# Performance work log

Hardware: AMD Instinct MI355X
Metric: run time of the kernel (lower is better)

Reference implementation:

```python
import jax, jax.numpy as jnp
from jax import lax
import numpy as np

T = 100  # number of binarization thresholds, as in nn.Module (linspace(0,1,100))
THRESHOLDS = jnp.linspace(0.0, 1.0, T)


def _count_components(binimg):
    """4-connected component count per image via iterative min-label propagation.
    binimg: [N,H,W] float in {0,1}. Returns [N] int32 component counts.
    Equivalent math to the source's recursive DFS flood fill, vectorized."""
    N, H, W = binimg.shape
    fg = binimg > 0
    BIG = H * W  # sentinel label for background
    idx = jnp.arange(H * W, dtype=jnp.int32).reshape(H, W)
    lab0 = jnp.where(fg, idx[None], jnp.int32(BIG))

    def prop(lab):
        p = jnp.pad(lab, ((0, 0), (1, 1), (1, 1)), constant_values=BIG)
        nmin = jnp.minimum(jnp.minimum(p[:, :-2, 1:-1], p[:, 2:, 1:-1]),
                           jnp.minimum(p[:, 1:-1, :-2], p[:, 1:-1, 2:]))
        return jnp.where(fg, jnp.minimum(lab, nmin), jnp.int32(BIG))

    def cond(c):
        return ~c[1]

    def body(c):
        lab = c[0]
        new = prop(prop(prop(lab)))  # 3 propagation steps per convergence check
        return (new, jnp.all(new == lab))

    lab, _ = lax.while_loop(cond, body, (lab0, jnp.array(False)))
    # each component keeps exactly one pixel whose label equals its own index
    return jnp.sum(fg & (lab == idx[None]), axis=(1, 2)).astype(jnp.int32)


def _betti(prob):
    """prob: [R,H,W] -> [T,R,2] (b0, b1) per threshold per region.
    b1 = b0 - euler, euler = #pixels - #4-neighbor edges (as in source)."""
    R, H, W = prob.shape
    binz = (prob[None] > THRESHOLDS[:, None, None, None]).astype(jnp.float32)  # [T,R,H,W]
    flat = binz.reshape(T * R, H, W)
    b0 = lax.stop_gradient(_count_components(flat)).astype(jnp.float32).reshape(T, R)
    pix = flat.sum((1, 2))
    edges = (flat[:, :-1] * flat[:, 1:]).sum((1, 2)) + (flat[:, :, :-1] * flat[:, :, 1:]).sum((1, 2))
    euler = (pix - edges).reshape(T, R)
    b1 = b0 - euler
    return jnp.stack([b0, b1], axis=-1)  # [T,R,2]


def setup_inputs() -> dict:
    key = jax.random.key(0)
    k1, k2 = jax.random.split(key)
    three_class_prob = jax.random.uniform(k1, (4, 3, 128, 128), dtype=jnp.float32)
    selected_regions = jnp.arange(4, dtype=jnp.int64)
    gt_barcodes = jax.random.uniform(k2, (4, 6, T - 1, 2), dtype=jnp.float32)
    return {"three_class_prob": three_class_prob,
            "selected_regions": selected_regions,
            "gt_barcodes": gt_barcodes}


def reference(three_class_prob, selected_regions, gt_barcodes):
    sel = three_class_prob[selected_regions]  # [R,3,H,W]
    inside = _betti(sel[:, 0])     # channel 0
    boundary = _betti(sel[:, 1])   # channel 1
    union = inside                 # source uses channel 0:1 again -> same values
    codes = jnp.concatenate([inside, boundary, union], axis=-1)  # [T,R,6]
    # barcode extraction: birth at increases of the betti curve, death at decreases
    d = codes[1:] - codes[:-1]                 # [T-1,R,6]
    th = THRESHOLDS[:-1, None, None]
    birth = jnp.where(d > 0, th, 0.0)
    death = jnp.where(d < 0, th, 0.0)
    barcodes = jnp.stack([birth, death], axis=-1).transpose(1, 2, 0, 3)  # [R,6,T-1,2]
    # fixed-shape matching: pair barcodes sorted by birth time (Hungarian surrogate)
    ord_b = jnp.argsort(barcodes[..., 0], axis=-1)
    ord_g = jnp.argsort(gt_barcodes[..., 0], axis=-1)
    bs = jnp.take_along_axis(barcodes, ord_b[..., None], axis=-2)
    gs = jnp.take_along_axis(gt_barcodes, ord_g[..., None], axis=-2)
    matched_diff = jnp.sum(jnp.abs(bs - gs), axis=-1)                  # [R,6,T-1]
    unmatched_len = jnp.sum(barcodes[..., 1] - barcodes[..., 0], axis=-1)  # [R,6]
    return jnp.mean(matched_diff) + jnp.mean(unmatched_len)
```

## Files before the change

kernel.cpp:

```cpp
#include <hip/hip_runtime.h>

typedef unsigned long long u64;

__device__ __forceinline__ int find_root(int* L, int a){
    int p = L[a];
    while(p != a){
        int gp = L[p];
        if(gp != p) L[a] = gp;
        a = p; p = gp;
    }
    return a;
}

__device__ __forceinline__ int unite(int* L, int a, int b){
    while(true){
        a = find_root(L, a);
        b = find_root(L, b);
        if(a == b) return 0;
        int hi = (a > b) ? a : b;
        int lo = (a > b) ? b : a;
        int old = atomicCAS(&L[hi], hi, lo);
        if(old == hi) return 1;
        a = old; b = lo;
    }
}

__global__ __launch_bounds__(256) void ccl_kernel(const float* __restrict__ prob,
                                                  const int*   __restrict__ sel,
                                                  float*       __restrict__ betti,
                                                  float*       __restrict__ out){
    __shared__ u64 M[256];
    __shared__ u64 S[256];
    __shared__ int Pr[257];
    __shared__ int L[8192];
    __shared__ int red[12];
    const int tid = threadIdx.x, bid = blockIdx.x;
    if(bid == 0 && tid == 0) atomicExch(out, 0.0f);
    const int ch = bid / 400, t = (bid % 400) >> 2, r = bid & 3;
    const float th = (float)t / 99.0f;
    const float* img = prob + (size_t)(sel[r] * 3 + ch) * 16384;

    const int lane = tid & 63, wave = tid >> 6;
    for(int c = 0; c < 64; c++){
        float v = img[c * 256 + wave * 64 + lane];
        u64 mm = __ballot(v > th);
        if(lane == 0) M[c * 4 + wave] = mm;
    }
    __syncthreads();

    const int w = tid, row = w >> 1, half = w & 1;
    const u64 m = M[w];
    const u64 lcar = half ? (M[w - 1] >> 63) : 0ULL;
    const u64 s = m & ~((m << 1) | lcar);
    S[w] = s;
    int pix   = __popcll(m);
    int edges = __popcll(m & ((m << 1) | lcar));
    const u64 va = (row > 0) ? M[w - 2] : 0ULL;
    edges += __popcll(m & va);
    const int runs = __popcll(s);

    int incl = runs;
    for(int off = 1; off < 64; off <<= 1){
        int n = __shfl_up(incl, off, 64);
        if(lane >= off) incl += n;
    }
    if(lane == 63) red[wave] = incl;
    __syncthreads();
    int woff = 0;
    for(int k = 0; k < wave; k++) woff += red[k];
    const int excl = woff + incl - runs;
    Pr[w] = excl;
    if(w == 255) Pr[256] = excl + runs;
    __syncthreads();
    const int R = Pr[256];

    {
        int4* L4 = (int4*)L;
        const int n4 = (R + 3) >> 2;
        for(int i = tid; i < n4; i += 256){ int b = i * 4; L4[i] = make_int4(b, b+1, b+2, b+3); }
    }
    __syncthreads();

    int merges = 0;
    if(row > 0){
        u64 c = m & va;
        if(c){
            const u64 ccar = half ? ((M[w - 1] & M[w - 3]) >> 63) : 0ULL;
            u64 cs = c & ~((c << 1) | ccar);
            if(cs){
                const u64 sa = S[w - 2];
                const int Pa = Pr[w - 2];
                do{
                    const int x = __ffsll(cs) - 1;
                    cs &= cs - 1;
                    const u64 lm = (2ULL << x) - 1;
                    const int nb = excl + __popcll(s  & lm) - 1;
                    const int na = Pa   + __popcll(sa & lm) - 1;
                    merges += unite(L, na, nb);
                }while(cs);
            }
        }
    }

    int v0 = pix, v1 = edges, v2 = merges;
    for(int off = 32; off; off >>= 1){
        v0 += __shfl_down(v0, off, 64);
        v1 += __shfl_down(v1, off, 64);
        v2 += __shfl_down(v2, off, 64);
    }
    __syncthreads();
    if(lane == 0){ red[wave*3] = v0; red[wave*3+1] = v1; red[wave*3+2] = v2; }
    __syncthreads();
    if(tid == 0){
        int P = 0, E = 0, MG = 0;
        for(int k = 0; k < 4; k++){ P += red[k*3]; E += red[k*3+1]; MG += red[k*3+2]; }
        const float b0f = (float)(R - MG);
        const float b1f = b0f - ((float)P - (float)E);
        const size_t o = (((size_t)ch * 100 + t) * 4 + r) * 2;
        betti[o] = b0f; betti[o + 1] = b1f;
    }
}

__global__ __launch_bounds__(128) void rows_kernel(const float* __restrict__ betti,
                                                   const float* __restrict__ gt,
                                                   float*       __restrict__ out){
    __shared__ float codes[100];
    __shared__ float birth[99], bs0[99], bs1[99], gs0[99], gs1[99];
    __shared__ float gsh[198];
    __shared__ float red[4];
    const int row = blockIdx.x;
    const int r = row / 6, j = row % 6;
    const int chmap[6] = {0, 0, 1, 1, 0, 0};
    const int ch = chmap[j], comp = j & 1;
    const int tid = threadIdx.x;

    if(tid < 100) codes[tid] = betti[(((size_t)ch * 100 + tid) * 4 + r) * 2 + comp];
    const float* g = gt + (size_t)row * 99 * 2;
    for(int i = tid; i < 198; i += 128) gsh[i] = g[i];
    __syncthreads();

    float b = 0.f, d = 0.f;
    if(tid < 99){
        const float dv = codes[tid + 1] - codes[tid];
        const float thv = (float)tid / 99.0f;
        b = (dv > 0.f) ? thv : 0.f;
        d = (dv < 0.f) ? thv : 0.f;
        birth[tid] = b;
    }
    __syncthreads();

    if(tid < 99){
        int zb = 0, tz = 0;
        for(int k = 0; k < 99; k++){
            const int z = (birth[k] == 0.f) ? 1 : 0;
            tz += z;
            if(k < tid) zb += z;
        }
        const int pos = (b == 0.f) ? zb : (tz + tid - zb);
        bs0[pos] = b; bs1[pos] = d;

        const float gb = gsh[tid * 2];
        int rank = 0;
        for(int k = 0; k < 99; k++){
            const float o = gsh[k * 2];
            rank += (o < gb || (o == gb && k < tid)) ? 1 : 0;
        }
        gs0[rank] = gb; gs1[rank] = gsh[tid * 2 + 1];
    }
    __syncthreads();

    float mm = 0.f, u = 0.f;
    if(tid < 99){
        mm = fabsf(bs0[tid] - gs0[tid]) + fabsf(bs1[tid] - gs1[tid]);
        u = d - b;
    }
    for(int off = 32; off; off >>= 1){
        mm += __shfl_down(mm, off, 64);
        u  += __shfl_down(u,  off, 64);
    }
    if((tid & 63) == 0){ red[(tid >> 6)*2] = mm; red[(tid >> 6)*2 + 1] = u; }
    __syncthreads();
    if(tid == 0)
        atomicAdd(out, (red[0] + red[2]) / 2376.0f + (red[1] + red[3]) / 24.0f);
}

extern "C" void kernel_launch(void* const* d_in, const int* in_sizes, int n_in,
                              void* d_out, int out_size, void* d_ws, size_t ws_size,
                              hipStream_t stream){
    const float* prob = (const float*)d_in[0];
    const int*   sel  = (const int*)d_in[1];
    const float* gt   = (const float*)d_in[2];
    float* betti = (float*)d_ws;

    ccl_kernel <<<800, 256, 0, stream>>>(prob, sel, betti, (float*)d_out);
    rows_kernel<<<24, 128, 0, stream>>>(betti, gt, (float*)d_out);
}
```

Baseline: 103.4 us.

## Replace CAS union-find with iterative atomicMin label propagation and pointer jumping

Removes the per-merge find/unite loops built on atomicCAS. Instead, each thread repeatedly hooks the vertical run adjacencies it owns with atomicMin. Every round is followed by a block-wide pointer-jumping pass and a shared 'changed' flag check. Components are counted as the labels that remain their own root, and the label array shrinks from 8192 to 6400 entries, which frees LDS for occupancy. The cost is an unknown number of block-synchronised rounds per image, plus the risk of overflow on images with more than 6400 runs.

Result: slower. 118.2 us (+14.3%).

```diff
diff --git a/kernel.cpp b/kernel.cpp
--- a/kernel.cpp
+++ b/kernel.cpp
@@ -1,29 +1,6 @@
 #include <hip/hip_runtime.h>
 
 typedef unsigned long long u64;
-
-__device__ __forceinline__ int find_root(int* L, int a){
-    int p = L[a];
-    while(p != a){
-        int gp = L[p];
-        if(gp != p) L[a] = gp;
-        a = p; p = gp;
-    }
-    return a;
-}
-
-__device__ __forceinline__ int unite(int* L, int a, int b){
-    while(true){
-        a = find_root(L, a);
-        b = find_root(L, b);
-        if(a == b) return 0;
-        int hi = (a > b) ? a : b;
-        int lo = (a > b) ? b : a;
-        int old = atomicCAS(&L[hi], hi, lo);
-        if(old == hi) return 1;
-        a = old; b = lo;
-    }
-}
 
 __global__ __launch_bounds__(256) void ccl_kernel(const float* __restrict__ prob,
                                                   const int*   __restrict__ sel,
@@ -32,8 +9,9 @@
     __shared__ u64 M[256];
     __shared__ u64 S[256];
     __shared__ int Pr[257];
-    __shared__ int L[8192];
+    __shared__ int L[6400];
     __shared__ int red[12];
+    __shared__ int changed;
     const int tid = threadIdx.x, bid = blockIdx.x;
     if(bid == 0 && tid == 0) atomicExch(out, 0.0f);
     const int ch = bid / 400, t = (bid % 400) >> 2, r = bid & 3;
@@ -58,6 +36,12 @@
     const u64 va = (row > 0) ? M[w - 2] : 0ULL;
     edges += __popcll(m & va);
     const int runs = __popcll(s);
+    u64 csm = 0ULL;
+    if(row > 0){
+        const u64 c = m & va;
+        const u64 ccar = half ? ((M[w - 1] & M[w - 3]) >> 63) : 0ULL;
+        csm = c & ~((c << 1) | ccar);
+    }
 
     int incl = runs;
     for(int off = 1; off < 64; off <<= 1){
@@ -71,38 +55,52 @@
     const int excl = woff + incl - runs;
     Pr[w] = excl;
     if(w == 255) Pr[256] = excl + runs;
+    const u64 sa = (row > 0) ? S[w - 2] : 0ULL;
     __syncthreads();
     const int R = Pr[256];
+    const int Pa = (row > 0) ? Pr[w - 2] : 0;
 
     {
         int4* L4 = (int4*)L;
         const int n4 = (R + 3) >> 2;
         for(int i = tid; i < n4; i += 256){ int b = i * 4; L4[i] = make_int4(b, b+1, b+2, b+3); }
     }
+    if(tid == 0) changed = 0;
     __syncthreads();
 
-    int merges = 0;
-    if(row > 0){
-        u64 c = m & va;
-        if(c){
-            const u64 ccar = half ? ((M[w - 1] & M[w - 3]) >> 63) : 0ULL;
-            u64 cs = c & ~((c << 1) | ccar);
-            if(cs){
-                const u64 sa = S[w - 2];
-                const int Pa = Pr[w - 2];
-                do{
-                    const int x = __ffsll(cs) - 1;
-                    cs &= cs - 1;
-                    const u64 lm = (2ULL << x) - 1;
-                    const int nb = excl + __popcll(s  & lm) - 1;
-                    const int na = Pa   + __popcll(sa & lm) - 1;
-                    merges += unite(L, na, nb);
-                }while(cs);
+    for(;;){
+        int chl = 0;
+        u64 cs = csm;
+        while(cs){
+            const int x = __ffsll(cs) - 1;
+            cs &= cs - 1;
+            const u64 lm = (2ULL << x) - 1;
+            const int nb = excl + __popcll(s  & lm) - 1;
+            const int na = Pa   + __popcll(sa & lm) - 1;
+            const int la = L[na], lb = L[nb];
+            if(la != lb){
+                const int hi = la > lb ? la : lb;
+                const int lo = la > lb ? lb : la;
+                atomicMin(&L[hi], lo);
+                chl = 1;
             }
         }
+        if(chl) changed = 1;
+        __syncthreads();
+        if(!changed) break;
+        for(int i = tid; i < R; i += 256){
+            const int p = L[i];
+            const int g = L[p];
+            if(g != p) L[i] = g;
+        }
+        if(tid == 0) changed = 0;
+        __syncthreads();
     }
 
-    int v0 = pix, v1 = edges, v2 = merges;
+    int rc = 0;
+    for(int i = tid; i < R; i += 256) rc += (L[i] == i);
+
+    int v0 = pix, v1 = edges, v2 = rc;
     for(int off = 32; off; off >>= 1){
         v0 += __shfl_down(v0, off, 64);
         v1 += __shfl_down(v1, off, 64);
@@ -112,9 +110,9 @@
     if(lane == 0){ red[wave*3] = v0; red[wave*3+1] = v1; red[wave*3+2] = v2; }
     __syncthreads();
     if(tid == 0){
-        int P = 0, E = 0, MG = 0;
-        for(int k = 0; k < 4; k++){ P += red[k*3]; E += red[k*3+1]; MG += red[k*3+2]; }
-        const float b0f = (float)(R - MG);
+        int P = 0, E = 0, B = 0;
+        for(int k = 0; k < 4; k++){ P += red[k*3]; E += red[k*3+1]; B += red[k*3+2]; }
+        const float b0f = (float)B;
         const float b1f = b0f - ((float)P - (float)E);
         const size_t o = (((size_t)ch * 100 + t) * 4 + r) * 2;
         betti[o] = b0f; betti[o + 1] = b1f;
```
